# Kernel tuning notes

Measured on AMD Instinct MI355X. Metric: run time of the kernel, lower is better.

Reference implementation:

```python
import jax, jax.numpy as jnp
import numpy as np

TOPK = 16  # module init arg
EPS = 1e-12  # F.normalize eps


def setup_inputs() -> dict:
    key = jax.random.key(0)
    k1, k2, k3 = jax.random.split(key, 3)
    b, c, h, w = 2, 256, 96, 96
    rc = max(c // 4, 16)  # reduced_channels = 64
    x = jax.random.normal(k1, (b, c, h, w), dtype=jnp.float32)
    # 1x1 convs are channel-mixing matmuls; store weights as [out_ch, in_ch]
    w_reduce = jax.random.normal(k2, (rc, c), dtype=jnp.float32) * 0.05
    w_proj = jax.random.normal(k3, (c, rc), dtype=jnp.float32) * 0.05
    return {"x": x, "w_reduce": w_reduce, "w_proj": w_proj}


def reference(x, w_reduce, w_proj):
    b, c, h, w = x.shape
    n = h * w
    # reduce: 1x1 conv == channel matmul -> [b, rc, N]
    feat = jnp.einsum('rc,bchw->brhw', w_reduce, x).reshape(b, -1, n)
    # F.normalize(dim=1): divide by max(L2-norm over channels, eps)
    nrm = jnp.maximum(jnp.sqrt(jnp.sum(feat * feat, axis=1, keepdims=True)), EPS)
    nf = jnp.transpose(feat / nrm, (0, 2, 1))  # [b, N, rc]
    # cosine similarity matrix [b, N, N]
    sim = jnp.einsum('bnr,bmr->bnm', nf, nf)
    k = min(TOPK, n)
    _, idx = jax.lax.top_k(sim, k)  # [b, N, k]
    # gather top-k neighbor features and average -> [b, N, rc]
    corr = jax.vmap(lambda f, i: f[i].mean(axis=1))(nf, idx)
    # proj: 1x1 conv back to C channels, NCHW layout
    enhanced = jnp.einsum('cr,bnr->bnc', w_proj, corr)
    enhanced = jnp.transpose(enhanced, (0, 2, 1)).reshape(b, c, h, w)
    return x + enhanced
```

## Files before the change

kernel.cpp:

```cpp
#include <hip/hip_runtime.h>
#include <cstdint>
#include <cstddef>

#define NPIX 9216
#define NB 2
#define NC 256
#define RC 64
#define TK 16
#define NROWS (NB * NPIX)
#define CT 128
#define ECOLS 1152
#define NTE 9
#define MAXC 128
#define MARGIN 0.008f

typedef unsigned short ushort_t;
typedef unsigned int uint_t;
typedef __bf16 bf16x8 __attribute__((ext_vector_type(8)));
typedef float f32x4 __attribute__((ext_vector_type(4)));

__device__ __forceinline__ uint_t f2bf(float x) {
  uint_t u = __float_as_uint(x);
  return (u + 0x7FFFu + ((u >> 16) & 1u)) >> 16;
}

__device__ __forceinline__ uint_t ordu(float v) {
  uint_t u = __float_as_uint(v);
  return (u & 0x80000000u) ? ~u : (u | 0x80000000u);
}

__global__ __launch_bounds__(256) void k_reduce(
    const float* __restrict__ x, const float* __restrict__ wr,
    float* __restrict__ feat4) {
  __shared__ float wl[64 * 16];
  const int bi = blockIdx.x;
  const int pg = bi >> 4, rq = (bi >> 2) & 3, cq = bi & 3;
  const int tid = threadIdx.x;
  {
    const int cl = tid >> 2, rg = (tid & 3) * 4;
#pragma unroll
    for (int i = 0; i < 4; ++i)
      wl[cl * 16 + rg + i] = wr[(size_t)(rq * 16 + rg + i) * NC + cq * 64 + cl];
  }
  __syncthreads();

  const int p = pg * 256 + tid;
  const int b = p >= NPIX;
  const int n = p - b * NPIX;
  const float* xp = x + (size_t)b * NC * NPIX + (size_t)cq * 64 * NPIX + n;

  float4 acc[4];
#pragma unroll
  for (int i = 0; i < 4; ++i) acc[i] = make_float4(0.f, 0.f, 0.f, 0.f);

  for (int c = 0; c < 64; ++c) {
    const float xv = xp[(size_t)c * NPIX];
    const float4* w4 = (const float4*)(wl + c * 16);
#pragma unroll
    for (int i = 0; i < 4; ++i) {
      float4 w = w4[i];
      acc[i].x += w.x * xv; acc[i].y += w.y * xv;
      acc[i].z += w.z * xv; acc[i].w += w.w * xv;
    }
  }
  float4* o = (float4*)(feat4 + (((size_t)(rq * 4 + cq)) * NROWS + p) * 16);
#pragma unroll
  for (int i = 0; i < 4; ++i) o[i] = acc[i];
}

__global__ __launch_bounds__(256) void k_normsplit(
    const float* __restrict__ feat4, float* __restrict__ nf,
    ushort_t* __restrict__ hi) {
  const int t = blockIdx.x * 256 + threadIdx.x;
  const int p = t >> 2, q = t & 3;
  float4 v[4];
#pragma unroll
  for (int i = 0; i < 4; ++i) v[i] = make_float4(0.f, 0.f, 0.f, 0.f);
#pragma unroll
  for (int pt = 0; pt < 4; ++pt) {
    const float4* fp = (const float4*)(feat4 + (((size_t)(q * 4 + pt)) * NROWS + p) * 16);
#pragma unroll
    for (int i = 0; i < 4; ++i) {
      float4 a = fp[i];
      v[i].x += a.x; v[i].y += a.y; v[i].z += a.z; v[i].w += a.w;
    }
  }
  float ssq = 0.f;
#pragma unroll
  for (int i = 0; i < 4; ++i)
    ssq += v[i].x * v[i].x + v[i].y * v[i].y + v[i].z * v[i].z + v[i].w * v[i].w;
  ssq += __shfl_xor(ssq, 1);
  ssq += __shfl_xor(ssq, 2);
  const float inv = 1.f / fmaxf(sqrtf(ssq), 1e-12f);

  float s[16];
#pragma unroll
  for (int i = 0; i < 4; ++i) {
    s[i * 4 + 0] = v[i].x * inv; s[i * 4 + 1] = v[i].y * inv;
    s[i * 4 + 2] = v[i].z * inv; s[i * 4 + 3] = v[i].w * inv;
  }
  float4* no = (float4*)(nf + (size_t)p * RC + q * 16);
#pragma unroll
  for (int i = 0; i < 4; ++i)
    no[i] = make_float4(s[i * 4], s[i * 4 + 1], s[i * 4 + 2], s[i * 4 + 3]);

  uint_t hs[16];
#pragma unroll
  for (int i = 0; i < 16; ++i) hs[i] = f2bf(s[i]);
  uint4* ho = (uint4*)(hi + (size_t)p * RC + q * 16);
#pragma unroll
  for (int h = 0; h < 2; ++h)
    ho[h] = make_uint4(hs[h*8+0] | (hs[h*8+1] << 16), hs[h*8+2] | (hs[h*8+3] << 16),
                       hs[h*8+4] | (hs[h*8+5] << 16), hs[h*8+6] | (hs[h*8+7] << 16));
}

__global__ __launch_bounds__(256) void k_sim_max(
    const ushort_t* __restrict__ nf_hi, float* __restrict__ tmax) {
  __shared__ ushort_t sh[CT * 72];
  const int rb = blockIdx.x >> 3, q = blockIdx.x & 7;
  const int tid = threadIdx.x, wave = tid >> 6, lane = tid & 63;
  const int n = lane & 15, quad = lane >> 4;
  const int r0 = rb * 128 + wave * 32 + n, r1 = r0 + 16;
  const int b = rb >= 72;
  const size_t cbase = (size_t)b * NPIX;

  const bf16x8 bh00 = *(const bf16x8*)(nf_hi + (size_t)r0 * 64 + quad * 8);
  const bf16x8 bh01 = *(const bf16x8*)(nf_hi + (size_t)r0 * 64 + 32 + quad * 8);
  const bf16x8 bh10 = *(const bf16x8*)(nf_hi + (size_t)r1 * 64 + quad * 8);
  const bf16x8 bh11 = *(const bf16x8*)(nf_hi + (size_t)r1 * 64 + 32 + quad * 8);

  const int sc = tid >> 1, sseg = (tid & 1) * 32;
  float cm0 = -1e30f, cm1 = -1e30f;

  for (int t = 0; t < NTE; ++t) {
    const int cb = q * ECOLS + t * CT;
    __syncthreads();
    {
      const uint4* g = (const uint4*)(nf_hi + (cbase + cb + sc) * 64 + sseg);
      uint4* d = (uint4*)(sh + sc * 72 + sseg);
#pragma unroll
      for (int i = 0; i < 4; ++i) d[i] = g[i];
    }
    __syncthreads();

#pragma unroll 2
    for (int st = 0; st < 8; ++st) {
      const ushort_t* ap = sh + (st * 16 + n) * 72 + quad * 8;
      bf16x8 ah0 = *(const bf16x8*)ap;
      bf16x8 ah1 = *(const bf16x8*)(ap + 32);
      f32x4 z = {0.f, 0.f, 0.f, 0.f};
      f32x4 a0 = __builtin_amdgcn_mfma_f32_16x16x32_bf16(ah0, bh00, z, 0, 0, 0);
      a0 = __builtin_amdgcn_mfma_f32_16x16x32_bf16(ah1, bh01, a0, 0, 0, 0);
      f32x4 a1 = __builtin_amdgcn_mfma_f32_16x16x32_bf16(ah0, bh10, z, 0, 0, 0);
      a1 = __builtin_amdgcn_mfma_f32_16x16x32_bf16(ah1, bh11, a1, 0, 0, 0);
      cm0 = fmaxf(cm0, fmaxf(fmaxf(a0[0], a0[1]), fmaxf(a0[2], a0[3])));
      cm1 = fmaxf(cm1, fmaxf(fmaxf(a1[0], a1[1]), fmaxf(a1[2], a1[3])));
    }
    if (t % 3 == 2) {
      const int cn = t / 3;
      tmax[(size_t)r0 * 96 + (q * 4 + quad) * 3 + cn] = cm0;
      tmax[(size_t)r1 * 96 + (q * 4 + quad) * 3 + cn] = cm1;
      cm0 = -1e30f; cm1 = -1e30f;
    }
  }
}

__global__ __launch_bounds__(256) void k_thresh(
    const float* __restrict__ tmax, float* __restrict__ Tb) {
  const int wave = threadIdx.x >> 6, lane = threadIdx.x & 63;
  const int row = blockIdx.x * 4 + wave;
  const float* tp = tmax + (size_t)row * 96;
  float v0 = tp[lane];
  float v1 = (lane < 32) ? tp[64 + lane] : -1e30f;
  float m = -1e30f;
#pragma unroll
  for (int k = 0; k < TK; ++k) {
    float c = fmaxf(v0, v1);
#pragma unroll
    for (int d = 1; d < 64; d <<= 1) c = fmaxf(c, __shfl_xor(c, d));
    m = c;
    if (v0 == m) v0 = -1e30f;
    if (v1 == m) v1 = -1e30f;
  }
  if (lane == 0) Tb[row] = m - MARGIN;
}

__global__ __launch_bounds__(256) void k_collect(
    const ushort_t* __restrict__ nf_hi, const float* __restrict__ Tb,
    int* __restrict__ cidx, int* __restrict__ rowcnt) {
  __shared__ ushort_t sh[CT * 72];
  const int rb = blockIdx.x >> 3, q = blockIdx.x & 7;
  const int tid = threadIdx.x, wave = tid >> 6, lane = tid & 63;
  const int n = lane & 15, quad = lane >> 4;
  const int r0 = rb * 128 + wave * 32 + n, r1 = r0 + 16;
  const int b = rb >= 72;
  const size_t cbase = (size_t)b * NPIX;

  const bf16x8 bh00 = *(const bf16x8*)(nf_hi + (size_t)r0 * 64 + quad * 8);
  const bf16x8 bh01 = *(const bf16x8*)(nf_hi + (size_t)r0 * 64 + 32 + quad * 8);
  const bf16x8 bh10 = *(const bf16x8*)(nf_hi + (size_t)r1 * 64 + quad * 8);
  const bf16x8 bh11 = *(const bf16x8*)(nf_hi + (size_t)r1 * 64 + 32 + quad * 8);

  const float T0 = Tb[r0], T1 = Tb[r1];
  const int sc = tid >> 1, sseg = (tid & 1) * 32;

  for (int t = 0; t < NTE; ++t) {
    const int cb = q * ECOLS + t * CT;
    __syncthreads();
    {
      const uint4* g = (const uint4*)(nf_hi + (cbase + cb + sc) * 64 + sseg);
      uint4* d = (uint4*)(sh + sc * 72 + sseg);
#pragma unroll
      for (int i = 0; i < 4; ++i) d[i] = g[i];
    }
    __syncthreads();

#pragma unroll 2
    for (int st = 0; st < 8; ++st) {
      const ushort_t* ap = sh + (st * 16 + n) * 72 + quad * 8;
      bf16x8 ah0 = *(const bf16x8*)ap;
      bf16x8 ah1 = *(const bf16x8*)(ap + 32);
      f32x4 z = {0.f, 0.f, 0.f, 0.f};
      f32x4 a0 = __builtin_amdgcn_mfma_f32_16x16x32_bf16(ah0, bh00, z, 0, 0, 0);
      a0 = __builtin_amdgcn_mfma_f32_16x16x32_bf16(ah1, bh01, a0, 0, 0, 0);
      f32x4 a1 = __builtin_amdgcn_mfma_f32_16x16x32_bf16(ah0, bh10, z, 0, 0, 0);
      a1 = __builtin_amdgcn_mfma_f32_16x16x32_bf16(ah1, bh11, a1, 0, 0, 0);

      const int c0 = cb + st * 16 + quad * 4;
      const float mx0 = fmaxf(fmaxf(a0[0], a0[1]), fmaxf(a0[2], a0[3]));
      if (mx0 >= T0) {
#pragma unroll
        for (int r = 0; r < 4; ++r)
          if (a0[r] >= T0) {
            const int slot = atomicAdd(rowcnt + r0, 1);
            if (slot < MAXC) cidx[(size_t)r0 * MAXC + slot] = c0 + r;
          }
      }
      const float mx1 = fmaxf(fmaxf(a1[0], a1[1]), fmaxf(a1[2], a1[3]));
      if (mx1 >= T1) {
#pragma unroll
        for (int r = 0; r < 4; ++r)
          if (a1[r] >= T1) {
            const int slot = atomicAdd(rowcnt + r1, 1);
            if (slot < MAXC) cidx[(size_t)r1 * MAXC + slot] = c0 + r;
          }
      }
    }
  }
}

__global__ __launch_bounds__(256) void k_merge_gather(
    const float* __restrict__ nf, const int* __restrict__ cidx,
    const int* __restrict__ rowcnt, float* __restrict__ corr) {
  const int wave = threadIdx.x >> 6, lane = threadIdx.x & 63;
  const int row0 = blockIdx.x * 16 + wave * 4;
#pragma unroll 1
  for (int rr = 0; rr < 4; ++rr) {
    const int row = row0 + rr;
    const int b = row >= NPIX;
    const int rl = row - b * NPIX;
    const float* nfb = nf + (size_t)b * NPIX * RC;
    const int C = min(rowcnt[row], MAXC);

    float4 rv[16];
    const float4* r4 = (const float4*)(nf + (size_t)row * RC);
#pragma unroll
    for (int i = 0; i < 16; ++i) rv[i] = r4[i];

    const int* cp = cidx + (size_t)row * MAXC;
    unsigned long long k0 = 0, k1 = 0;
    {
      const int c0 = (lane < C) ? cp[lane] : rl;
      const float4* g = (const float4*)(nfb + (size_t)c0 * RC);
      float s = 0.f;
#pragma unroll
      for (int i = 0; i < 16; ++i) {
        float4 a = g[i];
        s += a.x * rv[i].x + a.y * rv[i].y + a.z * rv[i].z + a.w * rv[i].w;
      }
      if (lane < C)
        k0 = ((unsigned long long)ordu(s) << 32) | (uint_t)(~(uint_t)c0);
    }
    if (C > 64) {
      const int c1 = (64 + lane < C) ? cp[64 + lane] : rl;
      const float4* g = (const float4*)(nfb + (size_t)c1 * RC);
      float s = 0.f;
#pragma unroll
      for (int i = 0; i < 16; ++i) {
        float4 a = g[i];
        s += a.x * rv[i].x + a.y * rv[i].y + a.z * rv[i].z + a.w * rv[i].w;
      }
      if (64 + lane < C)
        k1 = ((unsigned long long)ordu(s) << 32) | (uint_t)(~(uint_t)c1);
    }

    int sel[TK];
#pragma unroll
    for (int t = 0; t < TK; ++t) {
      unsigned long long m = k0 > k1 ? k0 : k1;
#pragma unroll
      for (int d = 1; d < 64; d <<= 1) {
        unsigned long long o = __shfl_xor(m, d);
        m = (o > m) ? o : m;
      }
      sel[t] = (m == 0) ? rl : (int)(~(uint_t)(m & 0xFFFFFFFFull));
      if (k0 == m) k0 = 0;
      else if (k1 == m) k1 = 0;
    }

    float acc = 0.f;
#pragma unroll
    for (int t = 0; t < TK; ++t)
      acc += nfb[(size_t)sel[t] * RC + lane];
    corr[(size_t)row * RC + lane] = acc * 0.0625f;
  }
}

__global__ __launch_bounds__(256) void k_proj_add(
    const float* __restrict__ x, const float* __restrict__ wp,
    const float* __restrict__ corr, float* __restrict__ out) {
  const int pg = blockIdx.x >> 3, cq = blockIdx.x & 7;
  const int tid = threadIdx.x;

  __shared__ float wl[32 * RC];
  {
    const float4* src = (const float4*)(wp + (size_t)cq * 32 * RC);
    float4* dst = (float4*)wl;
#pragma unroll
    for (int i = 0; i < 2; ++i) dst[i * 256 + tid] = src[i * 256 + tid];
  }

  const int p = pg * 256 + tid;
  const int b = p >= NPIX;
  const int n = p - b * NPIX;

  float4 cr[16];
  const float4* c4 = (const float4*)(corr + (size_t)p * RC);
#pragma unroll
  for (int i = 0; i < 16; ++i) cr[i] = c4[i];
  __syncthreads();

  const size_t xb = (size_t)b * NC * NPIX + n;
  for (int cl = 0; cl < 32; ++cl) {
    const float4* w4 = (const float4*)(wl + cl * RC);
    float s = 0.f;
#pragma unroll
    for (int i = 0; i < 16; ++i) {
      float4 w = w4[i];
      s += w.x * cr[i].x + w.y * cr[i].y + w.z * cr[i].z + w.w * cr[i].w;
    }
    const int c = cq * 32 + cl;
    const size_t oi = xb + (size_t)c * NPIX;
    out[oi] = x[oi] + s;
  }
}

extern "C" void kernel_launch(void* const* d_in, const int* in_sizes, int n_in,
                              void* d_out, int out_size, void* d_ws, size_t ws_size,
                              hipStream_t stream) {
  const float* x = (const float*)d_in[0];
  const float* wr = (const float*)d_in[1];
  const float* wp = (const float*)d_in[2];
  float* out = (float*)d_out;

  char* ws = (char*)d_ws;
  float* feat4 = (float*)ws;
  float* tmax = (float*)ws;
  float* corr = (float*)ws;
  float* nf = (float*)(ws + 18874368);
  ushort_t* nf_hi = (ushort_t*)(ws + 23592960);
  float* Tb = (float*)(ws + 25952256);
  int* rowcnt = (int*)(ws + 26025984);
  int* cidx = (int*)(ws + 26099712);

  hipLaunchKernelGGL(k_reduce, dim3(1152), dim3(256), 0, stream, x, wr, feat4);
  hipLaunchKernelGGL(k_normsplit, dim3(288), dim3(256), 0, stream, feat4, nf, nf_hi);
  hipLaunchKernelGGL(k_sim_max, dim3(1152), dim3(256), 0, stream, nf_hi, tmax);
  hipLaunchKernelGGL(k_thresh, dim3(NROWS / 4), dim3(256), 0, stream, tmax, Tb);
  hipMemsetAsync(rowcnt, 0, NROWS * sizeof(int), stream);
  hipLaunchKernelGGL(k_collect, dim3(1152), dim3(256), 0, stream,
                     nf_hi, Tb, cidx, rowcnt);
  hipLaunchKernelGGL(k_merge_gather, dim3(1152), dim3(256), 0, stream,
                     nf, cidx, rowcnt, corr);
  hipLaunchKernelGGL(k_proj_add, dim3(576), dim3(256), 0, stream, x, wp, corr, out);
}
```

Measured before the change: 314.9 us.

## Prefetch next column tile into registers, split columns 12 ways, one row per wave

The similarity-max and collect kernels now load the next 128-column tile into registers while MFMAs run on the current shared-memory tile, then write it to LDS between barriers. This overlaps global loads with compute. The column split rises from 8 to 12 chunks per row block, giving more, shorter blocks (tmax still holds 96 entries per row, now 12x4x2), which raises parallelism across CUs. The merge-gather kernel now assigns one row per wave instead of looping over four, launching four times as many blocks to improve latency hiding at the cost of extra block overhead.

```diff
diff --git a/kernel.cpp b/kernel.cpp
--- a/kernel.cpp
+++ b/kernel.cpp
@@ -9,8 +9,9 @@
 #define TK 16
 #define NROWS (NB * NPIX)
 #define CT 128
-#define ECOLS 1152
-#define NTE 9
+#define NQ 12
+#define ECOLS 768
+#define NTE 6
 #define MAXC 128
 #define MARGIN 0.008f
 
@@ -117,7 +118,7 @@
 __global__ __launch_bounds__(256) void k_sim_max(
     const ushort_t* __restrict__ nf_hi, float* __restrict__ tmax) {
   __shared__ ushort_t sh[CT * 72];
-  const int rb = blockIdx.x >> 3, q = blockIdx.x & 7;
+  const int rb = blockIdx.x / NQ, q = blockIdx.x % NQ;
   const int tid = threadIdx.x, wave = tid >> 6, lane = tid & 63;
   const int n = lane & 15, quad = lane >> 4;
   const int r0 = rb * 128 + wave * 32 + n, r1 = r0 + 16;
@@ -130,18 +131,112 @@
   const bf16x8 bh11 = *(const bf16x8*)(nf_hi + (size_t)r1 * 64 + 32 + quad * 8);
 
   const int sc = tid >> 1, sseg = (tid & 1) * 32;
+  uint4 stg[4];
+  {
+    const uint4* g = (const uint4*)(nf_hi + (cbase + q * ECOLS + sc) * 64 + sseg);
+#pragma unroll
+    for (int i = 0; i < 4; ++i) stg[i] = g[i];
+    uint4* d = (uint4*)(sh + sc * 72 + sseg);
+#pragma unroll
+    for (int i = 0; i < 4; ++i) d[i] = stg[i];
+  }
+  __syncthreads();
+
   float cm0 = -1e30f, cm1 = -1e30f;
+
+  for (int t = 0; t < NTE; ++t) {
+    if (t + 1 < NTE) {
+      const uint4* g = (const uint4*)(nf_hi + (cbase + q * ECOLS + (t + 1) * CT + sc) * 64 + sseg);
+#pragma unroll
+      for (int i = 0; i < 4; ++i) stg[i] = g[i];
+    }
+
+#pragma unroll 4
+    for (int st = 0; st < 8; ++st) {
+      const ushort_t* ap = sh + (st * 16 + n) * 72 + quad * 8;
+      bf16x8 ah0 = *(const bf16x8*)ap;
+      bf16x8 ah1 = *(const bf16x8*)(ap + 32);
+      f32x4 z = {0.f, 0.f, 0.f, 0.f};
+      f32x4 a0 = __builtin_amdgcn_mfma_f32_16x16x32_bf16(ah0, bh00, z, 0, 0, 0);
+      a0 = __builtin_amdgcn_mfma_f32_16x16x32_bf16(ah1, bh01, a0, 0, 0, 0);
+      f32x4 a1 = __builtin_amdgcn_mfma_f32_16x16x32_bf16(ah0, bh10, z, 0, 0, 0);
+      a1 = __builtin_amdgcn_mfma_f32_16x16x32_bf16(ah1, bh11, a1, 0, 0, 0);
+      cm0 = fmaxf(fmaxf(a0[0], a0[1]), fmaxf(fmaxf(a0[2], a0[3]), cm0));
+      cm1 = fmaxf(fmaxf(a1[0], a1[1]), fmaxf(fmaxf(a1[2], a1[3]), cm1));
+    }
+    if (t % 3 == 2) {
+      const int cn = t / 3;
+      tmax[(size_t)r0 * 96 + (q * 4 + quad) * 2 + cn] = cm0;
+      tmax[(size_t)r1 * 96 + (q * 4 + quad) * 2 + cn] = cm1;
+      cm0 = -1e30f; cm1 = -1e30f;
+    }
+    __syncthreads();
+    if (t + 1 < NTE) {
+      uint4* d = (uint4*)(sh + sc * 72 + sseg);
+#pragma unroll
+      for (int i = 0; i < 4; ++i) d[i] = stg[i];
+    }
+    __syncthreads();
+  }
+}
+
+__global__ __launch_bounds__(256) void k_thresh(
+    const float* __restrict__ tmax, float* __restrict__ Tb) {
+  const int wave = threadIdx.x >> 6, lane = threadIdx.x & 63;
+  const int row = blockIdx.x * 4 + wave;
+  const float* tp = tmax + (size_t)row * 96;
+  float v0 = tp[lane];
+  float v1 = (lane < 32) ? tp[64 + lane] : -1e30f;
+  float m = -1e30f;
+#pragma unroll
+  for (int k = 0; k < TK; ++k) {
+    float c = fmaxf(v0, v1);
+#pragma unroll
+    for (int d = 1; d < 64; d <<= 1) c = fmaxf(c, __shfl_xor(c, d));
+    m = c;
+    if (v0 == m) v0 = -1e30f;
+    if (v1 == m) v1 = -1e30f;
+  }
+  if (lane == 0) Tb[row] = m - MARGIN;
+}
+
+__global__ __launch_bounds__(256) void k_collect(
+    const ushort_t* __restrict__ nf_hi, const float* __restrict__ Tb,
+    int* __restrict__ cidx, int* __restrict__ rowcnt) {
+  __shared__ ushort_t sh[CT * 72];
+  const int rb = blockIdx.x / NQ, q = blockIdx.x % NQ;
+  const int tid = threadIdx.x, wave = tid >> 6, lane = tid & 63;
+  const int n = lane & 15, quad = lane >> 4;
+  const int r0 = rb * 128 + wave * 32 + n, r1 = r0 + 16;
+  const int b = rb >= 72;
+  const size_t cbase = (size_t)b * NPIX;
+
+  const bf16x8 bh00 = *(const bf16x8*)(nf_hi + (size_t)r0 * 64 + quad * 8);
+  const bf16x8 bh01 = *(const bf16x8*)(nf_hi + (size_t)r0 * 64 + 32 + quad * 8);
+  const bf16x8 bh10 = *(const bf16x8*)(nf_hi + (size_t)r1 * 64 + quad * 8);
+  const bf16x8 bh11 = *(const bf16x8*)(nf_hi + (size_t)r1 * 64 + 32 + quad * 8);
+
+  const float T0 = Tb[r0], T1 = Tb[r1];
+  const int sc = tid >> 1, sseg = (tid & 1) * 32;
+
+  uint4 stg[4];
+  {
+    const uint4* g = (const uint4*)(nf_hi + (cbase + q * ECOLS + sc) * 64 + sseg);
+#pragma unroll
+    for (int i = 0; i < 4; ++i) stg[i] = g[i];
+    uint4* d = (uint4*)(sh + sc * 72 + sseg);
+#pragma unroll
+    for (int i = 0; i < 4; ++i) d[i] = stg[i];
+  }
+  __syncthreads();
 
   for (int t = 0; t < NTE; ++t) {
     const int cb = q * ECOLS + t * CT;
-    __syncthreads();
-    {
-      const uint4* g = (const uint4*)(nf_hi + (cbase + cb + sc) * 64 + sseg);
-      uint4* d = (uint4*)(sh + sc * 72 + sseg);
-#pragma unroll
-      for (int i = 0; i < 4; ++i) d[i] = g[i];
-    }
-    __syncthreads();
+    if (t + 1 < NTE) {
+      const uint4* g = (const uint4*)(nf_hi + (cbase + cb + CT + sc) * 64 + sseg);
+#pragma unroll
+      for (int i = 0; i < 4; ++i) stg[i] = g[i];
+    }
 
 #pragma unroll 2
     for (int st = 0; st < 8; ++st) {
@@ -153,81 +248,9 @@
       a0 = __builtin_amdgcn_mfma_f32_16x16x32_bf16(ah1, bh01, a0, 0, 0, 0);
       f32x4 a1 = __builtin_amdgcn_mfma_f32_16x16x32_bf16(ah0, bh10, z, 0, 0, 0);
       a1 = __builtin_amdgcn_mfma_f32_16x16x32_bf16(ah1, bh11, a1, 0, 0, 0);
-      cm0 = fmaxf(cm0, fmaxf(fmaxf(a0[0], a0[1]), fmaxf(a0[2], a0[3])));
-      cm1 = fmaxf(cm1, fmaxf(fmaxf(a1[0], a1[1]), fmaxf(a1[2], a1[3])));
-    }
-    if (t % 3 == 2) {
-      const int cn = t / 3;
-      tmax[(size_t)r0 * 96 + (q * 4 + quad) * 3 + cn] = cm0;
-      tmax[(size_t)r1 * 96 + (q * 4 + quad) * 3 + cn] = cm1;
-      cm0 = -1e30f; cm1 = -1e30f;
-    }
-  }
-}
-
-__global__ __launch_bounds__(256) void k_thresh(
-    const float* __restrict__ tmax, float* __restrict__ Tb) {
-  const int wave = threadIdx.x >> 6, lane = threadIdx.x & 63;
-  const int row = blockIdx.x * 4 + wave;
-  const float* tp = tmax + (size_t)row * 96;
-  float v0 = tp[lane];
-  float v1 = (lane < 32) ? tp[64 + lane] : -1e30f;
-  float m = -1e30f;
-#pragma unroll
-  for (int k = 0; k < TK; ++k) {
-    float c = fmaxf(v0, v1);
-#pragma unroll
-    for (int d = 1; d < 64; d <<= 1) c = fmaxf(c, __shfl_xor(c, d));
-    m = c;
-    if (v0 == m) v0 = -1e30f;
-    if (v1 == m) v1 = -1e30f;
-  }
-  if (lane == 0) Tb[row] = m - MARGIN;
-}
-
-__global__ __launch_bounds__(256) void k_collect(
-    const ushort_t* __restrict__ nf_hi, const float* __restrict__ Tb,
-    int* __restrict__ cidx, int* __restrict__ rowcnt) {
-  __shared__ ushort_t sh[CT * 72];
-  const int rb = blockIdx.x >> 3, q = blockIdx.x & 7;
-  const int tid = threadIdx.x, wave = tid >> 6, lane = tid & 63;
-  const int n = lane & 15, quad = lane >> 4;
-  const int r0 = rb * 128 + wave * 32 + n, r1 = r0 + 16;
-  const int b = rb >= 72;
-  const size_t cbase = (size_t)b * NPIX;
-
-  const bf16x8 bh00 = *(const bf16x8*)(nf_hi + (size_t)r0 * 64 + quad * 8);
-  const bf16x8 bh01 = *(const bf16x8*)(nf_hi + (size_t)r0 * 64 + 32 + quad * 8);
-  const bf16x8 bh10 = *(const bf16x8*)(nf_hi + (size_t)r1 * 64 + quad * 8);
-  const bf16x8 bh11 = *(const bf16x8*)(nf_hi + (size_t)r1 * 64 + 32 + quad * 8);
-
-  const float T0 = Tb[r0], T1 = Tb[r1];
-  const int sc = tid >> 1, sseg = (tid & 1) * 32;
-
-  for (int t = 0; t < NTE; ++t) {
-    const int cb = q * ECOLS + t * CT;
-    __syncthreads();
-    {
-      const uint4* g = (const uint4*)(nf_hi + (cbase + cb + sc) * 64 + sseg);
-      uint4* d = (uint4*)(sh + sc * 72 + sseg);
-#pragma unroll
-      for (int i = 0; i < 4; ++i) d[i] = g[i];
-    }
-    __syncthreads();
-
-#pragma unroll 2
-    for (int st = 0; st < 8; ++st) {
-      const ushort_t* ap = sh + (st * 16 + n) * 72 + quad * 8;
-      bf16x8 ah0 = *(const bf16x8*)ap;
-      bf16x8 ah1 = *(const bf16x8*)(ap + 32);
-      f32x4 z = {0.f, 0.f, 0.f, 0.f};
-      f32x4 a0 = __builtin_amdgcn_mfma_f32_16x16x32_bf16(ah0, bh00, z, 0, 0, 0);
-      a0 = __builtin_amdgcn_mfma_f32_16x16x32_bf16(ah1, bh01, a0, 0, 0, 0);
-      f32x4 a1 = __builtin_amdgcn_mfma_f32_16x16x32_bf16(ah0, bh10, z, 0, 0, 0);
-      a1 = __builtin_amdgcn_mfma_f32_16x16x32_bf16(ah1, bh11, a1, 0, 0, 0);
 
       const int c0 = cb + st * 16 + quad * 4;
-      const float mx0 = fmaxf(fmaxf(a0[0], a0[1]), fmaxf(a0[2], a0[3]));
+      const float mx0 = fmaxf(fmaxf(fmaxf(a0[0], a0[1]), a0[2]), a0[3]);
       if (mx0 >= T0) {
 #pragma unroll
         for (int r = 0; r < 4; ++r)
@@ -236,7 +259,7 @@
             if (slot < MAXC) cidx[(size_t)r0 * MAXC + slot] = c0 + r;
           }
       }
-      const float mx1 = fmaxf(fmaxf(a1[0], a1[1]), fmaxf(a1[2], a1[3]));
+      const float mx1 = fmaxf(fmaxf(fmaxf(a1[0], a1[1]), a1[2]), a1[3]);
       if (mx1 >= T1) {
 #pragma unroll
         for (int r = 0; r < 4; ++r)
@@ -246,6 +269,13 @@
           }
       }
     }
+    __syncthreads();
+    if (t + 1 < NTE) {
+      uint4* d = (uint4*)(sh + sc * 72 + sseg);
+#pragma unroll
+      for (int i = 0; i < 4; ++i) d[i] = stg[i];
+    }
+    __syncthreads();
   }
 }
 
@@ -253,67 +283,63 @@
     const float* __restrict__ nf, const int* __restrict__ cidx,
     const int* __restrict__ rowcnt, float* __restrict__ corr) {
   const int wave = threadIdx.x >> 6, lane = threadIdx.x & 63;
-  const int row0 = blockIdx.x * 16 + wave * 4;
-#pragma unroll 1
-  for (int rr = 0; rr < 4; ++rr) {
-    const int row = row0 + rr;
-    const int b = row >= NPIX;
-    const int rl = row - b * NPIX;
-    const float* nfb = nf + (size_t)b * NPIX * RC;
-    const int C = min(rowcnt[row], MAXC);
-
-    float4 rv[16];
-    const float4* r4 = (const float4*)(nf + (size_t)row * RC);
-#pragma unroll
-    for (int i = 0; i < 16; ++i) rv[i] = r4[i];
-
-    const int* cp = cidx + (size_t)row * MAXC;
-    unsigned long long k0 = 0, k1 = 0;
-    {
-      const int c0 = (lane < C) ? cp[lane] : rl;
-      const float4* g = (const float4*)(nfb + (size_t)c0 * RC);
-      float s = 0.f;
-#pragma unroll
-      for (int i = 0; i < 16; ++i) {
-        float4 a = g[i];
-        s += a.x * rv[i].x + a.y * rv[i].y + a.z * rv[i].z + a.w * rv[i].w;
-      }
-      if (lane < C)
-        k0 = ((unsigned long long)ordu(s) << 32) | (uint_t)(~(uint_t)c0);
-    }
-    if (C > 64) {
-      const int c1 = (64 + lane < C) ? cp[64 + lane] : rl;
-      const float4* g = (const float4*)(nfb + (size_t)c1 * RC);
-      float s = 0.f;
-#pragma unroll
-      for (int i = 0; i < 16; ++i) {
-        float4 a = g[i];
-        s += a.x * rv[i].x + a.y * rv[i].y + a.z * rv[i].z + a.w * rv[i].w;
-      }
-      if (64 + lane < C)
-        k1 = ((unsigned long long)ordu(s) << 32) | (uint_t)(~(uint_t)c1);
-    }
-
-    int sel[TK];
-#pragma unroll
-    for (int t = 0; t < TK; ++t) {
-      unsigned long long m = k0 > k1 ? k0 : k1;
-#pragma unroll
-      for (int d = 1; d < 64; d <<= 1) {
-        unsigned long long o = __shfl_xor(m, d);
-        m = (o > m) ? o : m;
-      }
-      sel[t] = (m == 0) ? rl : (int)(~(uint_t)(m & 0xFFFFFFFFull));
-      if (k0 == m) k0 = 0;
-      else if (k1 == m) k1 = 0;
-    }
-
-    float acc = 0.f;
-#pragma unroll
-    for (int t = 0; t < TK; ++t)
-      acc += nfb[(size_t)sel[t] * RC + lane];
-    corr[(size_t)row * RC + lane] = acc * 0.0625f;
-  }
+  const int row = blockIdx.x * 4 + wave;
+  const int b = row >= NPIX;
+  const int rl = row - b * NPIX;
+  const float* nfb = nf + (size_t)b * NPIX * RC;
+  const int C = min(rowcnt[row], MAXC);
+
+  float4 rv[16];
+  const float4* r4 = (const float4*)(nf + (size_t)row * RC);
+#pragma unroll
+  for (int i = 0; i < 16; ++i) rv[i] = r4[i];
+
+  const int* cp = cidx + (size_t)row * MAXC;
+  unsigned long long k0 = 0, k1 = 0;
+  {
+    const int c0 = (lane < C) ? cp[lane] : rl;
+    const float4* g = (const float4*)(nfb + (size_t)c0 * RC);
+    float s = 0.f;
+#pragma unroll
+    for (int i = 0; i < 16; ++i) {
+      float4 a = g[i];
+      s += a.x * rv[i].x + a.y * rv[i].y + a.z * rv[i].z + a.w * rv[i].w;
+    }
+    if (lane < C)
+      k0 = ((unsigned long long)ordu(s) << 32) | (uint_t)(~(uint_t)c0);
+  }
+  if (C > 64) {
+    const int c1 = (64 + lane < C) ? cp[64 + lane] : rl;
+    const float4* g = (const float4*)(nfb + (size_t)c1 * RC);
+    float s = 0.f;
+#pragma unroll
+    for (int i = 0; i < 16; ++i) {
+      float4 a = g[i];
+      s += a.x * rv[i].x + a.y * rv[i].y + a.z * rv[i].z + a.w * rv[i].w;
+    }
+    if (64 + lane < C)
+      k1 = ((unsigned long long)ordu(s) << 32) | (uint_t)(~(uint_t)c1);
+  }
+
+  int sel[TK];
+#pragma unroll
+  for (int t = 0; t < TK; ++t) {
+    unsigned long long m = k0 > k1 ? k0 : k1;
+#pragma unroll
+    for (int d = 1; d < 64; d <<= 1) {
+      unsigned long long o = __shfl_xor(m, d);
+      m = (o > m) ? o : m;
+    }
+    sel[t] = (m == 0) ? rl : (int)(~(uint_t)(m & 0xFFFFFFFFull));
+    if (k0 == m) k0 = 0;
+    else if (k1 == m) k1 = 0;
+  }
+
+  float acc = 0.f;
+#pragma unroll
+  for (int t = 0; t < TK; ++t)
+    acc += nfb[(size_t)sel[t] * RC + lane];
+  corr[(size_t)row * RC + lane] = acc * 0.0625f;
 }
 
 __global__ __launch_bounds__(256) void k_proj_add(
@@ -375,12 +401,12 @@
 
   hipLaunchKernelGGL(k_reduce, dim3(1152), dim3(256), 0, stream, x, wr, feat4);
   hipLaunchKernelGGL(k_normsplit, dim3(288), dim3(256), 0, stream, feat4, nf, nf_hi);
-  hipLaunchKernelGGL(k_sim_max, dim3(1152), dim3(256), 0, stream, nf_hi, tmax);
+  hipLaunchKernelGGL(k_sim_max, dim3(144 * NQ), dim3(256), 0, stream, nf_hi, tmax);
   hipLaunchKernelGGL(k_thresh, dim3(NROWS / 4), dim3(256), 0, stream, tmax, Tb);
   hipMemsetAsync(rowcnt, 0, NROWS * sizeof(int), stream);
-  hipLaunchKernelGGL(k_collect, dim3(1152), dim3(256), 0, stream,
+  hipLaunchKernelGGL(k_collect, dim3(144 * NQ), dim3(256), 0, stream,
                      nf_hi, Tb, cidx, rowcnt);
-  hipLaunchKernelGGL(k_merge_gather, dim3(1152), dim3(256), 0, stream,
+  hipLaunchKernelGGL(k_merge_gather, dim3(NROWS / 4), dim3(256), 0, stream,
                      nf, cidx, rowcnt, corr);
   hipLaunchKernelGGL(k_proj_add, dim3(576), dim3(256), 0, stream, x, wp, corr, out);
 }
```

Measured after the change: 349.3 us. 10.9% more time.

## Double-buffer sim tiles via direct global-to-LDS loads with XOR swizzle

Applied to the files above, without the earlier changes.

The similarity-max and collect kernels now stage column tiles with global_load_lds into two LDS buffers, prefetching the next tile while MFMAs run on the current one. An XOR swizzle replaces the padded row layout to avoid bank conflicts. The collect kernel batches its per-element atomics into one atomicAdd per 4-value group, and merge_gather now uses one row per wave across more blocks for more parallelism. The risk is whether the async LDS loads are correctly fenced by the single barrier per iteration.

```diff
diff --git a/kernel.cpp b/kernel.cpp
--- a/kernel.cpp
+++ b/kernel.cpp
@@ -9,6 +9,7 @@
 #define TK 16
 #define NROWS (NB * NPIX)
 #define CT 128
+#define NQ 8
 #define ECOLS 1152
 #define NTE 9
 #define MAXC 128
@@ -27,6 +28,26 @@
 __device__ __forceinline__ uint_t ordu(float v) {
   uint_t u = __float_as_uint(v);
   return (u & 0x80000000u) ? ~u : (u | 0x80000000u);
+}
+
+#define GL2LDS(gsrc, ldst)                                                   \
+  __builtin_amdgcn_global_load_lds(                                          \
+      (const __attribute__((address_space(1))) uint_t*)(const void*)(gsrc),  \
+      (__attribute__((address_space(3))) uint_t*)(void*)(ldst), 16, 0, 0)
+
+__device__ __forceinline__ void stage_tile(
+    const ushort_t* __restrict__ nf_hi, size_t cbase, int cb,
+    ushort_t* shbuf, int tid) {
+  const int wave = tid >> 6, l = tid & 63;
+  const int lr = l >> 3;
+  const int ls = (l & 7) ^ lr;
+#pragma unroll
+  for (int i = 0; i < 4; ++i) {
+    const int j = wave * 4 + i;
+    const ushort_t* g = nf_hi + (cbase + (size_t)(cb + j * 8 + lr)) * 64 + ls * 8;
+    ushort_t* d = shbuf + j * 512;
+    GL2LDS(g, d);
+  }
 }
 
 __global__ __launch_bounds__(256) void k_reduce(
@@ -116,45 +137,44 @@
 
 __global__ __launch_bounds__(256) void k_sim_max(
     const ushort_t* __restrict__ nf_hi, float* __restrict__ tmax) {
-  __shared__ ushort_t sh[CT * 72];
+  __shared__ ushort_t sh[2][CT * 64];
   const int rb = blockIdx.x >> 3, q = blockIdx.x & 7;
   const int tid = threadIdx.x, wave = tid >> 6, lane = tid & 63;
   const int n = lane & 15, quad = lane >> 4;
   const int r0 = rb * 128 + wave * 32 + n, r1 = r0 + 16;
   const int b = rb >= 72;
   const size_t cbase = (size_t)b * NPIX;
+  const int x0 = (quad ^ (n & 7)) * 8;
+  const int x1 = ((quad + 4) ^ (n & 7)) * 8;
 
   const bf16x8 bh00 = *(const bf16x8*)(nf_hi + (size_t)r0 * 64 + quad * 8);
   const bf16x8 bh01 = *(const bf16x8*)(nf_hi + (size_t)r0 * 64 + 32 + quad * 8);
   const bf16x8 bh10 = *(const bf16x8*)(nf_hi + (size_t)r1 * 64 + quad * 8);
   const bf16x8 bh11 = *(const bf16x8*)(nf_hi + (size_t)r1 * 64 + 32 + quad * 8);
 
-  const int sc = tid >> 1, sseg = (tid & 1) * 32;
+  stage_tile(nf_hi, cbase, q * ECOLS, sh[0], tid);
+  __syncthreads();
+
   float cm0 = -1e30f, cm1 = -1e30f;
+  int cur = 0;
 
   for (int t = 0; t < NTE; ++t) {
-    const int cb = q * ECOLS + t * CT;
-    __syncthreads();
-    {
-      const uint4* g = (const uint4*)(nf_hi + (cbase + cb + sc) * 64 + sseg);
-      uint4* d = (uint4*)(sh + sc * 72 + sseg);
-#pragma unroll
-      for (int i = 0; i < 4; ++i) d[i] = g[i];
-    }
-    __syncthreads();
-
-#pragma unroll 2
+    if (t + 1 < NTE)
+      stage_tile(nf_hi, cbase, q * ECOLS + (t + 1) * CT, sh[cur ^ 1], tid);
+
+    const ushort_t* shc = sh[cur];
+#pragma unroll 4
     for (int st = 0; st < 8; ++st) {
-      const ushort_t* ap = sh + (st * 16 + n) * 72 + quad * 8;
-      bf16x8 ah0 = *(const bf16x8*)ap;
-      bf16x8 ah1 = *(const bf16x8*)(ap + 32);
+      const ushort_t* ap = shc + (st * 16 + n) * 64;
+      bf16x8 ah0 = *(const bf16x8*)(ap + x0);
+      bf16x8 ah1 = *(const bf16x8*)(ap + x1);
       f32x4 z = {0.f, 0.f, 0.f, 0.f};
       f32x4 a0 = __builtin_amdgcn_mfma_f32_16x16x32_bf16(ah0, bh00, z, 0, 0, 0);
       a0 = __builtin_amdgcn_mfma_f32_16x16x32_bf16(ah1, bh01, a0, 0, 0, 0);
       f32x4 a1 = __builtin_amdgcn_mfma_f32_16x16x32_bf16(ah0, bh10, z, 0, 0, 0);
       a1 = __builtin_amdgcn_mfma_f32_16x16x32_bf16(ah1, bh11, a1, 0, 0, 0);
-      cm0 = fmaxf(cm0, fmaxf(fmaxf(a0[0], a0[1]), fmaxf(a0[2], a0[3])));
-      cm1 = fmaxf(cm1, fmaxf(fmaxf(a1[0], a1[1]), fmaxf(a1[2], a1[3])));
+      cm0 = fmaxf(fmaxf(a0[0], a0[1]), fmaxf(fmaxf(a0[2], a0[3]), cm0));
+      cm1 = fmaxf(fmaxf(a1[0], a1[1]), fmaxf(fmaxf(a1[2], a1[3]), cm1));
     }
     if (t % 3 == 2) {
       const int cn = t / 3;
@@ -162,6 +182,8 @@
       tmax[(size_t)r1 * 96 + (q * 4 + quad) * 3 + cn] = cm1;
       cm0 = -1e30f; cm1 = -1e30f;
     }
+    __syncthreads();
+    cur ^= 1;
   }
 }
 
@@ -188,13 +210,15 @@
 __global__ __launch_bounds__(256) void k_collect(
     const ushort_t* __restrict__ nf_hi, const float* __restrict__ Tb,
     int* __restrict__ cidx, int* __restrict__ rowcnt) {
-  __shared__ ushort_t sh[CT * 72];
+  __shared__ ushort_t sh[2][CT * 64];
   const int rb = blockIdx.x >> 3, q = blockIdx.x & 7;
   const int tid = threadIdx.x, wave = tid >> 6, lane = tid & 63;
   const int n = lane & 15, quad = lane >> 4;
   const int r0 = rb * 128 + wave * 32 + n, r1 = r0 + 16;
   const int b = rb >= 72;
   const size_t cbase = (size_t)b * NPIX;
+  const int x0 = (quad ^ (n & 7)) * 8;
+  const int x1 = ((quad + 4) ^ (n & 7)) * 8;
 
   const bf16x8 bh00 = *(const bf16x8*)(nf_hi + (size_t)r0 * 64 + quad * 8);
   const bf16x8 bh01 = *(const bf16x8*)(nf_hi + (size_t)r0 * 64 + 32 + quad * 8);
@@ -202,24 +226,23 @@
   const bf16x8 bh11 = *(const bf16x8*)(nf_hi + (size_t)r1 * 64 + 32 + quad * 8);
 
   const float T0 = Tb[r0], T1 = Tb[r1];
-  const int sc = tid >> 1, sseg = (tid & 1) * 32;
+
+  stage_tile(nf_hi, cbase, q * ECOLS, sh[0], tid);
+  __syncthreads();
+
+  int cur = 0;
 
   for (int t = 0; t < NTE; ++t) {
     const int cb = q * ECOLS + t * CT;
-    __syncthreads();
-    {
-      const uint4* g = (const uint4*)(nf_hi + (cbase + cb + sc) * 64 + sseg);
-      uint4* d = (uint4*)(sh + sc * 72 + sseg);
-#pragma unroll
-      for (int i = 0; i < 4; ++i) d[i] = g[i];
-    }
-    __syncthreads();
-
+    if (t + 1 < NTE)
+      stage_tile(nf_hi, cbase, cb + CT, sh[cur ^ 1], tid);
+
+    const ushort_t* shc = sh[cur];
 #pragma unroll 2
     for (int st = 0; st < 8; ++st) {
-      const ushort_t* ap = sh + (st * 16 + n) * 72 + quad * 8;
-      bf16x8 ah0 = *(const bf16x8*)ap;
-      bf16x8 ah1 = *(const bf16x8*)(ap + 32);
+      const ushort_t* ap = shc + (st * 16 + n) * 64;
+      bf16x8 ah0 = *(const bf16x8*)(ap + x0);
+      bf16x8 ah1 = *(const bf16x8*)(ap + x1);
       f32x4 z = {0.f, 0.f, 0.f, 0.f};
       f32x4 a0 = __builtin_amdgcn_mfma_f32_16x16x32_bf16(ah0, bh00, z, 0, 0, 0);
       a0 = __builtin_amdgcn_mfma_f32_16x16x32_bf16(ah1, bh01, a0, 0, 0, 0);
@@ -227,25 +250,31 @@
       a1 = __builtin_amdgcn_mfma_f32_16x16x32_bf16(ah1, bh11, a1, 0, 0, 0);
 
       const int c0 = cb + st * 16 + quad * 4;
-      const float mx0 = fmaxf(fmaxf(a0[0], a0[1]), fmaxf(a0[2], a0[3]));
-      if (mx0 >= T0) {
+      const int m0 = (a0[0] >= T0) | ((a0[1] >= T0) << 1) |
+                     ((a0[2] >= T0) << 2) | ((a0[3] >= T0) << 3);
+      if (m0) {
+        int slot = atomicAdd(rowcnt + r0, __popc(m0));
 #pragma unroll
         for (int r = 0; r < 4; ++r)
-          if (a0[r] >= T0) {
-            const int slot = atomicAdd(rowcnt + r0, 1);
+          if (m0 & (1 << r)) {
             if (slot < MAXC) cidx[(size_t)r0 * MAXC + slot] = c0 + r;
+            ++slot;
           }
       }
-      const float mx1 = fmaxf(fmaxf(a1[0], a1[1]), fmaxf(a1[2], a1[3]));
-      if (mx1 >= T1) {
+      const int m1 = (a1[0] >= T1) | ((a1[1] >= T1) << 1) |
+                     ((a1[2] >= T1) << 2) | ((a1[3] >= T1) << 3);
+      if (m1) {
+        int slot = atomicAdd(rowcnt + r1, __popc(m1));
 #pragma unroll
         for (int r = 0; r < 4; ++r)
-          if (a1[r] >= T1) {
-            const int slot = atomicAdd(rowcnt + r1, 1);
+          if (m1 & (1 << r)) {
             if (slot < MAXC) cidx[(size_t)r1 * MAXC + slot] = c0 + r;
+            ++slot;
           }
       }
     }
+    __syncthreads();
+    cur ^= 1;
   }
 }
 
@@ -253,67 +282,63 @@
     const float* __restrict__ nf, const int* __restrict__ cidx,
     const int* __restrict__ rowcnt, float* __restrict__ corr) {
   const int wave = threadIdx.x >> 6, lane = threadIdx.x & 63;
-  const int row0 = blockIdx.x * 16 + wave * 4;
-#pragma unroll 1
-  for (int rr = 0; rr < 4; ++rr) {
-    const int row = row0 + rr;
-    const int b = row >= NPIX;
-    const int rl = row - b * NPIX;
-    const float* nfb = nf + (size_t)b * NPIX * RC;
-    const int C = min(rowcnt[row], MAXC);
-
-    float4 rv[16];
-    const float4* r4 = (const float4*)(nf + (size_t)row * RC);
-#pragma unroll
-    for (int i = 0; i < 16; ++i) rv[i] = r4[i];
-
-    const int* cp = cidx + (size_t)row * MAXC;
-    unsigned long long k0 = 0, k1 = 0;
-    {
-      const int c0 = (lane < C) ? cp[lane] : rl;
-      const float4* g = (const float4*)(nfb + (size_t)c0 * RC);
-      float s = 0.f;
-#pragma unroll
-      for (int i = 0; i < 16; ++i) {
-        float4 a = g[i];
-        s += a.x * rv[i].x + a.y * rv[i].y + a.z * rv[i].z + a.w * rv[i].w;
-      }
-      if (lane < C)
-        k0 = ((unsigned long long)ordu(s) << 32) | (uint_t)(~(uint_t)c0);
-    }
-    if (C > 64) {
-      const int c1 = (64 + lane < C) ? cp[64 + lane] : rl;
-      const float4* g = (const float4*)(nfb + (size_t)c1 * RC);
-      float s = 0.f;
-#pragma unroll
-      for (int i = 0; i < 16; ++i) {
-        float4 a = g[i];
-        s += a.x * rv[i].x + a.y * rv[i].y + a.z * rv[i].z + a.w * rv[i].w;
-      }
-      if (64 + lane < C)
-        k1 = ((unsigned long long)ordu(s) << 32) | (uint_t)(~(uint_t)c1);
-    }
-
-    int sel[TK];
-#pragma unroll
-    for (int t = 0; t < TK; ++t) {
-      unsigned long long m = k0 > k1 ? k0 : k1;
-#pragma unroll
-      for (int d = 1; d < 64; d <<= 1) {
-        unsigned long long o = __shfl_xor(m, d);
-        m = (o > m) ? o : m;
-      }
-      sel[t] = (m == 0) ? rl : (int)(~(uint_t)(m & 0xFFFFFFFFull));
-      if (k0 == m) k0 = 0;
-      else if (k1 == m) k1 = 0;
-    }
-
-    float acc = 0.f;
-#pragma unroll
-    for (int t = 0; t < TK; ++t)
-      acc += nfb[(size_t)sel[t] * RC + lane];
-    corr[(size_t)row * RC + lane] = acc * 0.0625f;
-  }
+  const int row = blockIdx.x * 4 + wave;
+  const int b = row >= NPIX;
+  const int rl = row - b * NPIX;
+  const float* nfb = nf + (size_t)b * NPIX * RC;
+  const int C = min(rowcnt[row], MAXC);
+
+  float4 rv[16];
+  const float4* r4 = (const float4*)(nf + (size_t)row * RC);
+#pragma unroll
+  for (int i = 0; i < 16; ++i) rv[i] = r4[i];
+
+  const int* cp = cidx + (size_t)row * MAXC;
+  unsigned long long k0 = 0, k1 = 0;
+  {
+    const int c0 = (lane < C) ? cp[lane] : rl;
+    const float4* g = (const float4*)(nfb + (size_t)c0 * RC);
+    float s = 0.f;
+#pragma unroll
+    for (int i = 0; i < 16; ++i) {
+      float4 a = g[i];
+      s += a.x * rv[i].x + a.y * rv[i].y + a.z * rv[i].z + a.w * rv[i].w;
+    }
+    if (lane < C)
+      k0 = ((unsigned long long)ordu(s) << 32) | (uint_t)(~(uint_t)c0);
+  }
+  if (C > 64) {
+    const int c1 = (64 + lane < C) ? cp[64 + lane] : rl;
+    const float4* g = (const float4*)(nfb + (size_t)c1 * RC);
+    float s = 0.f;
+#pragma unroll
+    for (int i = 0; i < 16; ++i) {
+      float4 a = g[i];
+      s += a.x * rv[i].x + a.y * rv[i].y + a.z * rv[i].z + a.w * rv[i].w;
+    }
+    if (64 + lane < C)
+      k1 = ((unsigned long long)ordu(s) << 32) | (uint_t)(~(uint_t)c1);
+  }
+
+  int sel[TK];
+#pragma unroll
+  for (int t = 0; t < TK; ++t) {
+    unsigned long long m = k0 > k1 ? k0 : k1;
+#pragma unroll
+    for (int d = 1; d < 64; d <<= 1) {
+      unsigned long long o = __shfl_xor(m, d);
+      m = (o > m) ? o : m;
+    }
+    sel[t] = (m == 0) ? rl : (int)(~(uint_t)(m & 0xFFFFFFFFull));
+    if (k0 == m) k0 = 0;
+    else if (k1 == m) k1 = 0;
+  }
+
+  float acc = 0.f;
+#pragma unroll
+  for (int t = 0; t < TK; ++t)
+    acc += nfb[(size_t)sel[t] * RC + lane];
+  corr[(size_t)row * RC + lane] = acc * 0.0625f;
 }
 
 __global__ __launch_bounds__(256) void k_proj_add(
@@ -380,7 +405,7 @@
   hipMemsetAsync(rowcnt, 0, NROWS * sizeof(int), stream);
   hipLaunchKernelGGL(k_collect, dim3(1152), dim3(256), 0, stream,
                      nf_hi, Tb, cidx, rowcnt);
-  hipLaunchKernelGGL(k_merge_gather, dim3(1152), dim3(256), 0, stream,
+  hipLaunchKernelGGL(k_merge_gather, dim3(NROWS / 4), dim3(256), 0, stream,
                      nf, cidx, rowcnt, corr);
   hipLaunchKernelGGL(k_proj_add, dim3(576), dim3(256), 0, stream, x, wp, corr, out);
 }
```

Measured after the change: 348.2 us. 1.11x slower.
